# Performance work log

Hardware: AMD Instinct MI355X
Metric: run time of the kernel (lower is better)

## Reference

```python
import jax, jax.numpy as jnp
import numpy as np

CURV_BOUNDS = (-2.0, 2.0)
THRESH = 0.01   # |k| below this -> Euclidean branch
EPS = 1e-5

B, S, D = 4, 2048, 512


def setup_inputs() -> dict:
    key = jax.random.key(0)
    ks = jax.random.split(key, 8)
    x = jax.random.normal(ks[0], (B, S, D), jnp.float32)
    sc = 1.0 / np.sqrt(D)  # ~ nn.Linear default init scale
    Wq = jax.random.uniform(ks[1], (D, D), jnp.float32, -sc, sc)
    bq = jax.random.uniform(ks[2], (D,), jnp.float32, -sc, sc)
    Wk = jax.random.uniform(ks[3], (D, D), jnp.float32, -sc, sc)
    bk = jax.random.uniform(ks[4], (D,), jnp.float32, -sc, sc)
    Wv = jax.random.uniform(ks[5], (D, D), jnp.float32, -sc, sc)
    bv = jax.random.uniform(ks[6], (D,), jnp.float32, -sc, sc)
    curvature_raw = jnp.float32(0.5)   # init_curvature
    temperature = jnp.float32(1.0)
    mask = jnp.triu(jnp.ones((S, S), dtype=bool), 1)  # causal: True = masked out
    return {"x": x, "Wq": Wq, "bq": bq, "Wk": Wk, "bk": bk, "Wv": Wv,
            "bv": bv, "curvature_raw": curvature_raw,
            "temperature": temperature, "mask": mask}


def _curvature(raw):
    k_min, k_max = CURV_BOUNDS
    return k_min + (k_max - k_min) * (jnp.tanh(raw) + 1.0) / 2.0


def _project(u, k):
    # project_to_manifold: identity (euclid), Poincare-ball clip (k<0), sphere renorm (k>0)
    n = jnp.sqrt(jnp.sum(u * u, axis=-1, keepdims=True) + 1e-12)
    absk = jnp.abs(k)
    sk = jnp.sqrt(jnp.maximum(absk, EPS))
    max_norm = (1.0 - 1e-3) / sk                      # ball radius 1/sqrt(|k|)
    u_hyp = u * jnp.minimum(1.0, max_norm / n)
    u_sph = u / (n * sk)                              # sphere radius 1/sqrt(k)
    return jnp.where(absk < THRESH, u, jnp.where(k < 0, u_hyp, u_sph))


def reference(x, Wq, bq, Wk, bk, Wv, bv, curvature_raw, temperature, mask):
    k = _curvature(curvature_raw)
    q = x @ Wq.T + bq
    kk = x @ Wk.T + bk
    v = x @ Wv.T + bv
    qm = _project(q, k)
    km = _project(kk, k)

    # pairwise quantities without materializing [B,S,S,D]
    dots = jnp.einsum('bid,bjd->bij', qm, km)         # [B,S,S]
    qn2 = jnp.sum(qm * qm, axis=-1)                   # [B,S]
    kn2 = jnp.sum(km * km, axis=-1)                   # [B,S]
    diff2 = jnp.maximum(qn2[:, :, None] + kn2[:, None, :] - 2.0 * dots, 0.0)

    absk = jnp.abs(k)
    sk = jnp.sqrt(jnp.maximum(absk, EPS))

    d_euc = jnp.sqrt(diff2 + 1e-12)
    # hyperbolic (Poincare ball, c=|k|): acosh(1 + 2c|x-y|^2 / ((1-c|x|^2)(1-c|y|^2))) / sqrt(c)
    denom = jnp.maximum((1.0 - absk * qn2)[:, :, None] * (1.0 - absk * kn2)[:, None, :], EPS)
    arg = 1.0 + 2.0 * absk * diff2 / denom
    d_hyp = jnp.arccosh(jnp.maximum(arg, 1.0 + 1e-7)) / sk
    # spherical (radius 1/sqrt(k)): arccos(k * <x,y>) / sqrt(k)
    cosang = jnp.clip(absk * dots, -1.0 + 1e-7, 1.0 - 1e-7)
    d_sph = jnp.arccos(cosang) / sk

    dist = jnp.where(absk < THRESH, d_euc, jnp.where(k < 0, d_hyp, d_sph))

    scores = -dist / (temperature + 1e-8)
    scores = jnp.where(mask[None, :, :], -jnp.inf, scores)
    attention = jax.nn.softmax(scores, axis=-1)       # [B,S,S]
    output = jnp.einsum('bij,bjd->bid', attention, v) # [B,S,D]
    return output, attention
```

## Files before the change

kernel.cpp:

```cpp
#include <hip/hip_runtime.h>
#include <hip/hip_bf16.h>
#include <math.h>

typedef unsigned short u16;
typedef float float4e __attribute__((ext_vector_type(4)));
typedef short short8 __attribute__((ext_vector_type(8)));
typedef unsigned short ushort8 __attribute__((ext_vector_type(8)));
typedef unsigned short u16x4 __attribute__((ext_vector_type(4)));

#define SEQ 2048
#define DIM 512
#define NB  4

__device__ __forceinline__ float bf2f(u16 h) {
    return __uint_as_float(((unsigned)h) << 16);
}
__device__ __forceinline__ u16 f2bf(float f) {
    __hip_bfloat16 h = __float2bfloat16(f);
    return *reinterpret_cast<u16*>(&h);
}
__device__ __forceinline__ float curv_of(float raw) {
    return -2.0f + 2.0f * (tanhf(raw) + 1.0f);
}
__device__ __forceinline__ void gl_lds16(const u16* g, u16* lds) {
    __builtin_amdgcn_global_load_lds(
        (const __attribute__((address_space(1))) unsigned int*)g,
        (__attribute__((address_space(3))) unsigned int*)lds, 16, 0, 0);
}

__global__ __launch_bounds__(256) void cvt_all_kernel(
    const float* __restrict__ x, const float* __restrict__ Wq,
    const float* __restrict__ Wk, const float* __restrict__ Wv,
    u16* __restrict__ x_bf, u16* __restrict__ Wcat, float* __restrict__ lsum)
{
    const int n_x = NB * SEQ * DIM, n_w = DIM * DIM;
    int gid = blockIdx.x * 256 + threadIdx.x;
    if (gid < NB * SEQ) lsum[gid] = 0.f;
    int i4 = gid * 4;
    if (i4 < n_x) {
        float4 v = *(const float4*)&x[i4];
        u16x4 h = {f2bf(v.x), f2bf(v.y), f2bf(v.z), f2bf(v.w)};
        *(u16x4*)&x_bf[i4] = h;
    } else if (i4 < n_x + 3 * n_w) {
        int j = i4 - n_x;
        const float* W = (j < n_w) ? Wq : (j < 2 * n_w ? Wk : Wv);
        int off = j % n_w;
        float4 v = *(const float4*)&W[off];
        u16x4 h = {f2bf(v.x), f2bf(v.y), f2bf(v.z), f2bf(v.w)};
        *(u16x4*)&Wcat[j] = h;
    }
}

__global__ __launch_bounds__(256, 2) void gemm_qkv_kernel(
    const u16* __restrict__ A, const u16* __restrict__ Bt,
    u16* __restrict__ C, u16* __restrict__ vT,
    const float* __restrict__ bq, const float* __restrict__ bk, const float* __restrict__ bv)
{
    const int lda = 512, ldb = 512, ldc = 1536;
    int bn = blockIdx.x, bm = blockIdx.y;

    __shared__ __align__(16) u16 As[128 * 64];
    __shared__ __align__(16) u16 Bs[128 * 64];

    int t = threadIdx.x, wave = t >> 6, lane = t & 63;
    int wr = wave >> 1, wc = wave & 1;
    int lrow = lane & 15, quad = lane >> 4;
    int srow = lane >> 3, sc8 = lane & 7;

    const u16* Ab = A + (size_t)(bm * 128) * lda;
    const u16* Bb = Bt + (size_t)(bn * 128) * ldb;

    float4e acc[4][4];
#pragma unroll
    for (int i = 0; i < 4; i++)
#pragma unroll
        for (int j = 0; j < 4; j++) acc[i][j] = (float4e){0.f, 0.f, 0.f, 0.f};

    for (int kt = 0; kt < 8; ++kt) {
        int k0 = kt << 6;
        __syncthreads();
#pragma unroll
        for (int h = 0; h < 4; ++h) {
            int q = wave * 4 + h;
            int row = q * 8 + srow;
            int c = sc8 ^ (row & 7);
            gl_lds16(Ab + (size_t)row * lda + k0 + c * 8, &As[q * 512]);
            gl_lds16(Bb + (size_t)row * ldb + k0 + c * 8, &Bs[q * 512]);
        }
        __syncthreads();
#pragma unroll
        for (int kk = 0; kk < 2; ++kk) {
            short8 af[4], bfr[4];
#pragma unroll
            for (int im = 0; im < 4; im++) {
                int R = wr * 64 + im * 16 + lrow;
                af[im] = *(const short8*)&As[R * 64 + (((kk * 4 + quad) ^ (R & 7)) * 8)];
            }
#pragma unroll
            for (int in = 0; in < 4; in++) {
                int R = wc * 64 + in * 16 + lrow;
                bfr[in] = *(const short8*)&Bs[R * 64 + (((kk * 4 + quad) ^ (R & 7)) * 8)];
            }
#pragma unroll
            for (int im = 0; im < 4; im++)
#pragma unroll
                for (int in = 0; in < 4; in++)
                    acc[im][in] = __builtin_amdgcn_mfma_f32_16x16x32_bf16(af[im], bfr[in], acc[im][in], 0, 0, 0);
        }
    }

#pragma unroll
    for (int in = 0; in < 4; in++) {
        int gj = bn * 128 + wc * 64 + in * 16 + lrow;
        float bias = (gj < 512) ? bq[gj] : (gj < 1024 ? bk[gj - 512] : bv[gj - 1024]);
#pragma unroll
        for (int im = 0; im < 4; im++) {
            int gi0 = bm * 128 + wr * 64 + im * 16 + quad * 4;
            u16x4 pack;
#pragma unroll
            for (int r = 0; r < 4; r++) {
                u16 hv = f2bf(acc[im][in][r] + bias);
                C[(size_t)(gi0 + r) * ldc + gj] = hv;
                pack[r] = hv;
            }
            if (gj >= 1024) {
                int bb = gi0 >> 11, s = gi0 & 2047;
                *(u16x4*)&vT[((size_t)bb * DIM + (gj - 1024)) * SEQ + s] = pack;
            }
        }
    }
}

__global__ __launch_bounds__(256, 4) void gemm_scores_kernel(
    const u16* __restrict__ qm, const u16* __restrict__ km,
    u16* __restrict__ attnH,
    float* __restrict__ lsum,
    const float* __restrict__ qn2v, const float* __restrict__ kn2v,
    const float* __restrict__ curvp, const float* __restrict__ tempp)
{
    const int lda = 512, ldb = 512, ldc = SEQ;
    int bn = blockIdx.x, bm = blockIdx.y, b = blockIdx.z;
    if (bn > 2 * bm + 1) return;

    __shared__ __align__(16) u16 As[128 * 64];
    __shared__ __align__(16) u16 Bs[64 * 64];

    int t = threadIdx.x, wave = t >> 6, lane = t & 63;
    int wr = wave >> 1, wc = wave & 1;
    int lrow = lane & 15, quad = lane >> 4;
    int srow = lane >> 3, sc8 = lane & 7;

    const u16* Ab = qm + (size_t)b * SEQ * DIM + (size_t)(bm * 128) * lda;
    const u16* Bb = km + (size_t)b * SEQ * DIM + (size_t)(bn * 64) * ldb;

    float4e acc[4][2];
#pragma unroll
    for (int i = 0; i < 4; i++)
#pragma unroll
        for (int j = 0; j < 2; j++) acc[i][j] = (float4e){0.f, 0.f, 0.f, 0.f};

    for (int kt = 0; kt < 8; ++kt) {
        int k0 = kt << 6;
        __syncthreads();
#pragma unroll
        for (int h = 0; h < 4; ++h) {
            int q = wave * 4 + h;
            int row = q * 8 + srow;
            int c = sc8 ^ (row & 7);
            gl_lds16(Ab + (size_t)row * lda + k0 + c * 8, &As[q * 512]);
        }
#pragma unroll
        for (int h = 0; h < 2; ++h) {
            int q = wave * 2 + h;
            int row = q * 8 + srow;
            int c = sc8 ^ (row & 7);
            gl_lds16(Bb + (size_t)row * ldb + k0 + c * 8, &Bs[q * 512]);
        }
        __syncthreads();
#pragma unroll
        for (int kk = 0; kk < 2; ++kk) {
            short8 af[4], bfr[2];
#pragma unroll
            for (int im = 0; im < 4; im++) {
                int R = wr * 64 + im * 16 + lrow;
                af[im] = *(const short8*)&As[R * 64 + (((kk * 4 + quad) ^ (R & 7)) * 8)];
            }
#pragma unroll
            for (int in = 0; in < 2; in++) {
                int R = wc * 32 + in * 16 + lrow;
                bfr[in] = *(const short8*)&Bs[R * 64 + (((kk * 4 + quad) ^ (R & 7)) * 8)];
            }
#pragma unroll
            for (int im = 0; im < 4; im++)
#pragma unroll
                for (int in = 0; in < 2; in++)
                    acc[im][in] = __builtin_amdgcn_mfma_f32_16x16x32_bf16(af[im], bfr[in], acc[im][in], 0, 0, 0);
        }
    }

    float kv = curv_of(curvp[0]);
    float absk = fabsf(kv);
    float sk = sqrtf(fmaxf(absk, 1e-5f));
    float invT = 1.0f / (tempp[0] + 1e-8f);
    float Cexp = -1.4426950408889634f * invT;
    u16* Cb = attnH + (size_t)b * SEQ * SEQ;

    float psum[4][4];
#pragma unroll
    for (int im = 0; im < 4; im++)
#pragma unroll
        for (int r = 0; r < 4; r++) psum[im][r] = 0.f;

    float kn[2];
#pragma unroll
    for (int in = 0; in < 2; in++)
        kn[in] = kn2v[b * SEQ + bn * 64 + wc * 32 + in * 16 + lrow];

#pragma unroll
    for (int im = 0; im < 4; im++) {
#pragma unroll
        for (int r = 0; r < 4; r++) {
            int gi = bm * 128 + wr * 64 + im * 16 + quad * 4 + r;
            float qn = qn2v[b * SEQ + gi];
#pragma unroll
            for (int in = 0; in < 2; in++) {
                int gj = bn * 64 + wc * 32 + in * 16 + lrow;
                float dot = acc[im][in][r];
                float diff2 = fmaxf(qn + kn[in] - 2.f * dot, 0.f);
                float dist;
                if (absk < 0.01f) {
                    dist = sqrtf(diff2 + 1e-12f);
                } else if (kv < 0.f) {
                    float denom = fmaxf((1.f - absk * qn) * (1.f - absk * kn[in]), 1e-5f);
                    float arg = fmaxf(1.f + 2.f * absk * diff2 / denom, 1.f + 1e-7f);
                    dist = acoshf(arg) / sk;
                } else {
                    float c = fminf(fmaxf(absk * dot, -1.f + 1e-7f), 1.f - 1e-7f);
                    dist = acosf(c) / sk;
                }
                float e = (gj <= gi) ? exp2f(dist * Cexp) : 0.f;
                Cb[(size_t)gi * ldc + gj] = f2bf(e);
                psum[im][r] += e;
            }
        }
    }
#pragma unroll
    for (int im = 0; im < 4; im++)
#pragma unroll
        for (int r = 0; r < 4; r++) {
            float v = psum[im][r];
            v += __shfl_xor(v, 1);
            v += __shfl_xor(v, 2);
            v += __shfl_xor(v, 4);
            v += __shfl_xor(v, 8);
            if (lrow == 0) {
                int gi = bm * 128 + wr * 64 + im * 16 + quad * 4 + r;
                atomicAdd(&lsum[b * SEQ + gi], v);
            }
        }
}

__global__ __launch_bounds__(256, 8) void gemm_pv_kernel(
    const u16* __restrict__ attnH, const u16* __restrict__ vT,
    float* __restrict__ out, const float* __restrict__ lsum)
{
    const int lda = SEQ, ldb = SEQ, ldc = DIM;
    int bn = blockIdx.x, bm = blockIdx.y, b = blockIdx.z;

    __shared__ __align__(16) u16 As[64 * 64];
    __shared__ __align__(16) u16 Bs[64 * 64];

    int t = threadIdx.x, wave = t >> 6, lane = t & 63;
    int wr = wave >> 1, wc = wave & 1;
    int lrow = lane & 15, quad = lane >> 4;
    int srow = lane >> 3, sc = lane & 7;

    const u16* Ab = attnH + (size_t)b * SEQ * SEQ + (size_t)(bm * 64) * lda;
    const u16* Bb = vT + (size_t)b * DIM * SEQ + (size_t)(bn * 64) * ldb;

    float4e acc[2][2];
#pragma unroll
    for (int i = 0; i < 2; i++)
#pragma unroll
        for (int j = 0; j < 2; j++) acc[i][j] = (float4e){0.f, 0.f, 0.f, 0.f};

    for (int kt = 0; kt <= bm; ++kt) {
        int k0 = kt << 6;
        __syncthreads();
#pragma unroll
        for (int h = 0; h < 2; ++h) {
            int q = wave * 2 + h;
            int row = q * 8 + srow;
            int c = sc ^ (row & 7);
            gl_lds16(Ab + (size_t)row * lda + k0 + c * 8, &As[q * 512]);
            gl_lds16(Bb + (size_t)row * ldb + k0 + c * 8, &Bs[q * 512]);
        }
        __syncthreads();
#pragma unroll
        for (int s = 0; s < 2; ++s) {
            short8 af[2], bfr[2];
#pragma unroll
            for (int im = 0; im < 2; im++) {
                int R = wr * 32 + im * 16 + lrow;
                af[im] = *(const short8*)&As[R * 64 + (((s * 4 + quad) ^ (R & 7)) * 8)];
            }
#pragma unroll
            for (int in = 0; in < 2; in++) {
                int R = wc * 32 + in * 16 + lrow;
                bfr[in] = *(const short8*)&Bs[R * 64 + (((s * 4 + quad) ^ (R & 7)) * 8)];
            }
#pragma unroll
            for (int im = 0; im < 2; im++)
#pragma unroll
                for (int in = 0; in < 2; in++)
                    acc[im][in] = __builtin_amdgcn_mfma_f32_16x16x32_bf16(af[im], bfr[in], acc[im][in], 0, 0, 0);
        }
    }

    float* Cb = out + (size_t)b * SEQ * DIM;
#pragma unroll
    for (int im = 0; im < 2; im++)
#pragma unroll
        for (int r = 0; r < 4; r++) {
            int gi = bm * 64 + wr * 32 + im * 16 + quad * 4 + r;
            float invl = 1.0f / lsum[b * SEQ + gi];
#pragma unroll
            for (int in = 0; in < 2; in++) {
                int gd = bn * 64 + wc * 32 + in * 16 + lrow;
                Cb[(size_t)gi * ldc + gd] = acc[im][in][r] * invl;
            }
        }
}

__global__ __launch_bounds__(256) void project_kernel(
    const u16* __restrict__ qkvh,
    u16* __restrict__ qm, u16* __restrict__ km,
    float* __restrict__ qn2, float* __restrict__ kn2,
    const float* __restrict__ curvp)
{
    int wave = threadIdx.x >> 6, lane = threadIdx.x & 63;
    int r = blockIdx.x * 4 + wave;
    float kv = curv_of(curvp[0]);
    float absk = fabsf(kv);
    float sk = sqrtf(fmaxf(absk, 1e-5f));

    const u16* qrow = qkvh + (size_t)r * 1536;
    ushort8 qh = *(const ushort8*)&qrow[lane * 8];
    ushort8 kh = *(const ushort8*)&qrow[512 + lane * 8];

    float qv[8], kw[8];
    float sq = 0.f, s2 = 0.f;
#pragma unroll
    for (int e = 0; e < 8; e++) {
        qv[e] = bf2f(qh[e]); sq += qv[e] * qv[e];
        kw[e] = bf2f(kh[e]); s2 += kw[e] * kw[e];
    }
#pragma unroll
    for (int off = 1; off < 64; off <<= 1) {
        sq += __shfl_xor(sq, off);
        s2 += __shfl_xor(s2, off);
    }

    float sclq, sclk;
    {
        float nq = sqrtf(sq + 1e-12f);
        float nk = sqrtf(s2 + 1e-12f);
        if (absk < 0.01f) { sclq = 1.f; sclk = 1.f; }
        else if (kv < 0.f) {
            float mx = (1.0f - 1e-3f) / sk;
            sclq = fminf(1.f, mx / nq);
            sclk = fminf(1.f, mx / nk);
        } else {
            sclq = 1.f / (nq * sk);
            sclk = 1.f / (nk * sk);
        }
    }
    if (lane == 0) {
        qn2[r] = sq * sclq * sclq;
        kn2[r] = s2 * sclk * sclk;
    }
    ushort8 qo, ko;
#pragma unroll
    for (int e = 0; e < 8; e++) {
        qo[e] = f2bf(qv[e] * sclq);
        ko[e] = f2bf(kw[e] * sclk);
    }
    *(ushort8*)&qm[(size_t)r * 512 + lane * 8] = qo;
    *(ushort8*)&km[(size_t)r * 512 + lane * 8] = ko;
}

__global__ __launch_bounds__(256) void norm_attn_kernel(
    const u16* __restrict__ attnH, const float* __restrict__ lsum,
    float* __restrict__ attnF)
{
    int i = blockIdx.x, b = blockIdx.y, t = threadIdx.x;
    float inv = 1.0f / lsum[b * SEQ + i];
    const u16* rowh = attnH + ((size_t)b * SEQ + i) * SEQ;
    float* row = attnF + ((size_t)b * SEQ + i) * SEQ;
    int L = i + 1;
    int j0 = t * 8;
    float4 lo, hi;
    if (j0 + 8 <= L) {
        ushort8 h = *(const ushort8*)&rowh[j0];
        lo.x = bf2f(h[0]) * inv; lo.y = bf2f(h[1]) * inv;
        lo.z = bf2f(h[2]) * inv; lo.w = bf2f(h[3]) * inv;
        hi.x = bf2f(h[4]) * inv; hi.y = bf2f(h[5]) * inv;
        hi.z = bf2f(h[6]) * inv; hi.w = bf2f(h[7]) * inv;
    } else {
        float v[8];
#pragma unroll
        for (int e = 0; e < 8; e++)
            v[e] = (j0 + e < L) ? bf2f(rowh[j0 + e]) * inv : 0.f;
        lo = (float4){v[0], v[1], v[2], v[3]};
        hi = (float4){v[4], v[5], v[6], v[7]};
    }
    *(float4*)&row[j0] = lo;
    *(float4*)&row[j0 + 4] = hi;
}

extern "C" void kernel_launch(void* const* d_in, const int* in_sizes, int n_in,
                              void* d_out, int out_size, void* d_ws, size_t ws_size,
                              hipStream_t stream) {
    (void)in_sizes; (void)n_in; (void)out_size; (void)ws_size;

    const float* x    = (const float*)d_in[0];
    const float* Wq   = (const float*)d_in[1];
    const float* bq   = (const float*)d_in[2];
    const float* Wk   = (const float*)d_in[3];
    const float* bk   = (const float*)d_in[4];
    const float* Wv   = (const float*)d_in[5];
    const float* bv   = (const float*)d_in[6];
    const float* curv = (const float*)d_in[7];
    const float* temp = (const float*)d_in[8];

    float* out   = (float*)d_out;
    float* attnF = out + (size_t)NB * SEQ * DIM;

    char* ws = (char*)d_ws;
    u16*   x_bf  = (u16*)(ws + 0);
    u16*   Wcat  = (u16*)(ws + 8388608);
    u16*   qkvh  = (u16*)(ws + 9961472);
    u16*   qm    = (u16*)(ws + 35127296);
    u16*   km    = (u16*)(ws + 43515904);
    u16*   vT    = (u16*)(ws + 51904512);
    float* qn2   = (float*)(ws + 60293120);
    float* kn2   = (float*)(ws + 60325888);
    float* lsum  = (float*)(ws + 60358656);
    u16*   attnH = (u16*)(ws + 0);

    {
        int n_tot = (NB * SEQ * DIM + 3 * DIM * DIM) / 4;
        cvt_all_kernel<<<(n_tot + 255) / 256, 256, 0, stream>>>(x, Wq, Wk, Wv, x_bf, Wcat, lsum);
    }

    gemm_qkv_kernel<<<dim3(1536 / 128, 8192 / 128, 1), 256, 0, stream>>>(
        x_bf, Wcat, qkvh, vT, bq, bk, bv);

    project_kernel<<<NB * SEQ / 4, 256, 0, stream>>>(qkvh, qm, km, qn2, kn2, curv);

    gemm_scores_kernel<<<dim3(SEQ / 64, SEQ / 128, NB), 256, 0, stream>>>(
        qm, km, attnH, lsum, qn2, kn2, curv, temp);

    gemm_pv_kernel<<<dim3(DIM / 64, SEQ / 64, NB), 256, 0, stream>>>(
        attnH, vT, out, lsum);

    norm_attn_kernel<<<dim3(SEQ, NB), 256, 0, stream>>>(attnH, lsum, attnF);
}
```

Baseline: 239.9 us.

## Fuse projection into QKV/score GEMMs and attention normalization into PV kernel

Removes the separate project kernel. QKV GEMM epilogue now writes q and k directly and accumulates their row squared norms with atomics, and the manifold scaling is applied in the scores epilogue by rescaling the dot products. The score tile grows to 128x128 with occupancy hint reduced. The norm_attn kernel is folded into the PV kernel, which writes the normalized fp32 attention from LDS tiles and zero-fills the masked upper region. This trades extra launches and memory passes for atomics, a heavier PV epilogue and a changed rounding point (bf16 of unscaled q/k).

```diff
diff --git a/kernel.cpp b/kernel.cpp
--- a/kernel.cpp
+++ b/kernel.cpp
@@ -31,11 +31,12 @@
 __global__ __launch_bounds__(256) void cvt_all_kernel(
     const float* __restrict__ x, const float* __restrict__ Wq,
     const float* __restrict__ Wk, const float* __restrict__ Wv,
-    u16* __restrict__ x_bf, u16* __restrict__ Wcat, float* __restrict__ lsum)
+    u16* __restrict__ x_bf, u16* __restrict__ Wcat,
+    float* __restrict__ lsum, float* __restrict__ qn2r, float* __restrict__ kn2r)
 {
     const int n_x = NB * SEQ * DIM, n_w = DIM * DIM;
     int gid = blockIdx.x * 256 + threadIdx.x;
-    if (gid < NB * SEQ) lsum[gid] = 0.f;
+    if (gid < NB * SEQ) { lsum[gid] = 0.f; qn2r[gid] = 0.f; kn2r[gid] = 0.f; }
     int i4 = gid * 4;
     if (i4 < n_x) {
         float4 v = *(const float4*)&x[i4];
@@ -53,10 +54,11 @@
 
 __global__ __launch_bounds__(256, 2) void gemm_qkv_kernel(
     const u16* __restrict__ A, const u16* __restrict__ Bt,
-    u16* __restrict__ C, u16* __restrict__ vT,
-    const float* __restrict__ bq, const float* __restrict__ bk, const float* __restrict__ bv)
+    u16* __restrict__ qbuf, u16* __restrict__ kbuf, u16* __restrict__ vT,
+    const float* __restrict__ bq, const float* __restrict__ bk, const float* __restrict__ bv,
+    float* __restrict__ qn2r, float* __restrict__ kn2r)
 {
-    const int lda = 512, ldb = 512, ldc = 1536;
+    const int lda = 512, ldb = 512;
     int bn = blockIdx.x, bm = blockIdx.y;
 
     __shared__ __align__(16) u16 As[128 * 64];
@@ -109,6 +111,13 @@
         }
     }
 
+    int region = bn >> 2;
+    float nsum[4][4];
+#pragma unroll
+    for (int im = 0; im < 4; im++)
+#pragma unroll
+        for (int r = 0; r < 4; r++) nsum[im][r] = 0.f;
+
 #pragma unroll
     for (int in = 0; in < 4; in++) {
         int gj = bn * 128 + wc * 64 + in * 16 + lrow;
@@ -120,44 +129,63 @@
 #pragma unroll
             for (int r = 0; r < 4; r++) {
                 u16 hv = f2bf(acc[im][in][r] + bias);
-                C[(size_t)(gi0 + r) * ldc + gj] = hv;
                 pack[r] = hv;
-            }
-            if (gj >= 1024) {
+                if (region == 0) {
+                    qbuf[(size_t)(gi0 + r) * 512 + gj] = hv;
+                } else if (region == 1) {
+                    kbuf[(size_t)(gi0 + r) * 512 + (gj - 512)] = hv;
+                }
+                if (region < 2) { float vv = bf2f(hv); nsum[im][r] += vv * vv; }
+            }
+            if (region == 2) {
                 int bb = gi0 >> 11, s = gi0 & 2047;
                 *(u16x4*)&vT[((size_t)bb * DIM + (gj - 1024)) * SEQ + s] = pack;
             }
         }
     }
-}
-
-__global__ __launch_bounds__(256, 4) void gemm_scores_kernel(
-    const u16* __restrict__ qm, const u16* __restrict__ km,
-    u16* __restrict__ attnH,
-    float* __restrict__ lsum,
-    const float* __restrict__ qn2v, const float* __restrict__ kn2v,
+    if (region < 2) {
+        float* nrm = (region == 0) ? qn2r : kn2r;
+#pragma unroll
+        for (int im = 0; im < 4; im++)
+#pragma unroll
+            for (int r = 0; r < 4; r++) {
+                float v = nsum[im][r];
+                v += __shfl_xor(v, 1);
+                v += __shfl_xor(v, 2);
+                v += __shfl_xor(v, 4);
+                v += __shfl_xor(v, 8);
+                if (lrow == 0)
+                    atomicAdd(&nrm[bm * 128 + wr * 64 + im * 16 + quad * 4 + r], v);
+            }
+    }
+}
+
+__global__ __launch_bounds__(256, 2) void gemm_scores_kernel(
+    const u16* __restrict__ qbuf, const u16* __restrict__ kbuf,
+    u16* __restrict__ attnH, float* __restrict__ lsum,
+    const float* __restrict__ qn2r, const float* __restrict__ kn2r,
     const float* __restrict__ curvp, const float* __restrict__ tempp)
 {
     const int lda = 512, ldb = 512, ldc = SEQ;
     int bn = blockIdx.x, bm = blockIdx.y, b = blockIdx.z;
-    if (bn > 2 * bm + 1) return;
+    if (bn > bm) return;
 
     __shared__ __align__(16) u16 As[128 * 64];
-    __shared__ __align__(16) u16 Bs[64 * 64];
+    __shared__ __align__(16) u16 Bs[128 * 64];
 
     int t = threadIdx.x, wave = t >> 6, lane = t & 63;
     int wr = wave >> 1, wc = wave & 1;
     int lrow = lane & 15, quad = lane >> 4;
     int srow = lane >> 3, sc8 = lane & 7;
 
-    const u16* Ab = qm + (size_t)b * SEQ * DIM + (size_t)(bm * 128) * lda;
-    const u16* Bb = km + (size_t)b * SEQ * DIM + (size_t)(bn * 64) * ldb;
-
-    float4e acc[4][2];
+    const u16* Ab = qbuf + (size_t)(b * SEQ + bm * 128) * lda;
+    const u16* Bb = kbuf + (size_t)(b * SEQ + bn * 128) * ldb;
+
+    float4e acc[4][4];
 #pragma unroll
     for (int i = 0; i < 4; i++)
 #pragma unroll
-        for (int j = 0; j < 2; j++) acc[i][j] = (float4e){0.f, 0.f, 0.f, 0.f};
+        for (int j = 0; j < 4; j++) acc[i][j] = (float4e){0.f, 0.f, 0.f, 0.f};
 
     for (int kt = 0; kt < 8; ++kt) {
         int k0 = kt << 6;
@@ -168,32 +196,26 @@
             int row = q * 8 + srow;
             int c = sc8 ^ (row & 7);
             gl_lds16(Ab + (size_t)row * lda + k0 + c * 8, &As[q * 512]);
-        }
-#pragma unroll
-        for (int h = 0; h < 2; ++h) {
-            int q = wave * 2 + h;
-            int row = q * 8 + srow;
-            int c = sc8 ^ (row & 7);
             gl_lds16(Bb + (size_t)row * ldb + k0 + c * 8, &Bs[q * 512]);
         }
         __syncthreads();
 #pragma unroll
         for (int kk = 0; kk < 2; ++kk) {
-            short8 af[4], bfr[2];
+            short8 af[4], bfr[4];
 #pragma unroll
             for (int im = 0; im < 4; im++) {
                 int R = wr * 64 + im * 16 + lrow;
                 af[im] = *(const short8*)&As[R * 64 + (((kk * 4 + quad) ^ (R & 7)) * 8)];
             }
 #pragma unroll
-            for (int in = 0; in < 2; in++) {
-                int R = wc * 32 + in * 16 + lrow;
+            for (int in = 0; in < 4; in++) {
+                int R = wc * 64 + in * 16 + lrow;
                 bfr[in] = *(const short8*)&Bs[R * 64 + (((kk * 4 + quad) ^ (R & 7)) * 8)];
             }
 #pragma unroll
             for (int im = 0; im < 4; im++)
 #pragma unroll
-                for (int in = 0; in < 2; in++)
+                for (int in = 0; in < 4; in++)
                     acc[im][in] = __builtin_amdgcn_mfma_f32_16x16x32_bf16(af[im], bfr[in], acc[im][in], 0, 0, 0);
         }
     }
@@ -201,37 +223,46 @@
     float kv = curv_of(curvp[0]);
     float absk = fabsf(kv);
     float sk = sqrtf(fmaxf(absk, 1e-5f));
+    bool euc = (absk < 0.01f);
+    float mxn = (1.0f - 1e-3f) / sk;
     float invT = 1.0f / (tempp[0] + 1e-8f);
     float Cexp = -1.4426950408889634f * invT;
     u16* Cb = attnH + (size_t)b * SEQ * SEQ;
 
+    float sclk[4], knp[4];
+#pragma unroll
+    for (int in = 0; in < 4; in++) {
+        float kr = kn2r[b * SEQ + bn * 128 + wc * 64 + in * 16 + lrow];
+        float nk = sqrtf(kr + 1e-12f);
+        float s = euc ? 1.f : (kv < 0.f ? fminf(1.f, mxn / nk) : 1.f / (nk * sk));
+        sclk[in] = s; knp[in] = kr * s * s;
+    }
+
     float psum[4][4];
 #pragma unroll
     for (int im = 0; im < 4; im++)
 #pragma unroll
         for (int r = 0; r < 4; r++) psum[im][r] = 0.f;
-
-    float kn[2];
-#pragma unroll
-    for (int in = 0; in < 2; in++)
-        kn[in] = kn2v[b * SEQ + bn * 64 + wc * 32 + in * 16 + lrow];
 
 #pragma unroll
     for (int im = 0; im < 4; im++) {
 #pragma unroll
         for (int r = 0; r < 4; r++) {
             int gi = bm * 128 + wr * 64 + im * 16 + quad * 4 + r;
-            float qn = qn2v[b * SEQ + gi];
-#pragma unroll
-            for (int in = 0; in < 2; in++) {
-                int gj = bn * 64 + wc * 32 + in * 16 + lrow;
-                float dot = acc[im][in][r];
-                float diff2 = fmaxf(qn + kn[in] - 2.f * dot, 0.f);
+            float qr = qn2r[b * SEQ + gi];
+            float nq = sqrtf(qr + 1e-12f);
+            float sq_ = euc ? 1.f : (kv < 0.f ? fminf(1.f, mxn / nq) : 1.f / (nq * sk));
+            float qn = qr * sq_ * sq_;
+#pragma unroll
+            for (int in = 0; in < 4; in++) {
+                int gj = bn * 128 + wc * 64 + in * 16 + lrow;
+                float dot = acc[im][in][r] * sq_ * sclk[in];
+                float diff2 = fmaxf(qn + knp[in] - 2.f * dot, 0.f);
                 float dist;
-                if (absk < 0.01f) {
+                if (euc) {
                     dist = sqrtf(diff2 + 1e-12f);
                 } else if (kv < 0.f) {
-                    float denom = fmaxf((1.f - absk * qn) * (1.f - absk * kn[in]), 1e-5f);
+                    float denom = fmaxf((1.f - absk * qn) * (1.f - absk * knp[in]), 1e-5f);
                     float arg = fmaxf(1.f + 2.f * absk * diff2 / denom, 1.f + 1e-7f);
                     dist = acoshf(arg) / sk;
                 } else {
@@ -260,9 +291,10 @@
         }
 }
 
-__global__ __launch_bounds__(256, 8) void gemm_pv_kernel(
+__global__ __launch_bounds__(256, 4) void gemm_pv_kernel(
     const u16* __restrict__ attnH, const u16* __restrict__ vT,
-    float* __restrict__ out, const float* __restrict__ lsum)
+    float* __restrict__ out, float* __restrict__ attnF,
+    const float* __restrict__ lsum)
 {
     const int lda = SEQ, ldb = SEQ, ldc = DIM;
     int bn = blockIdx.x, bm = blockIdx.y, b = blockIdx.z;
@@ -277,6 +309,18 @@
 
     const u16* Ab = attnH + (size_t)b * SEQ * SEQ + (size_t)(bm * 64) * lda;
     const u16* Bb = vT + (size_t)b * DIM * SEQ + (size_t)(bn * 64) * ldb;
+    float* attnFb = attnF + (size_t)b * SEQ * SEQ;
+
+    {
+        int r = t >> 2, c4 = t & 3;
+        float4 z = (float4){0.f, 0.f, 0.f, 0.f};
+        for (int kt = bm + 1; kt < 32; ++kt)
+            if ((kt & 7) == bn) {
+                float* dst = attnFb + (size_t)(bm * 64 + r) * SEQ + kt * 64 + c4 * 16;
+                ((float4*)dst)[0] = z; ((float4*)dst)[1] = z;
+                ((float4*)dst)[2] = z; ((float4*)dst)[3] = z;
+            }
+    }
 
     float4e acc[2][2];
 #pragma unroll
@@ -315,6 +359,22 @@
                 for (int in = 0; in < 2; in++)
                     acc[im][in] = __builtin_amdgcn_mfma_f32_16x16x32_bf16(af[im], bfr[in], acc[im][in], 0, 0, 0);
         }
+        if ((kt & 7) == bn) {
+            int r = t >> 2, c4 = t & 3;
+            int gi = bm * 64 + r;
+            float invl = 1.0f / lsum[b * SEQ + gi];
+            const u16* src = &As[r * 64];
+            int j0 = c4 * 2;
+            ushort8 u0 = *(const ushort8*)&src[(j0 ^ (r & 7)) * 8];
+            ushort8 u1 = *(const ushort8*)&src[((j0 + 1) ^ (r & 7)) * 8];
+            float* dst = attnFb + (size_t)gi * SEQ + kt * 64 + c4 * 16;
+            float4 f0 = {bf2f(u0[0]) * invl, bf2f(u0[1]) * invl, bf2f(u0[2]) * invl, bf2f(u0[3]) * invl};
+            float4 f1 = {bf2f(u0[4]) * invl, bf2f(u0[5]) * invl, bf2f(u0[6]) * invl, bf2f(u0[7]) * invl};
+            float4 f2 = {bf2f(u1[0]) * invl, bf2f(u1[1]) * invl, bf2f(u1[2]) * invl, bf2f(u1[3]) * invl};
+            float4 f3 = {bf2f(u1[4]) * invl, bf2f(u1[5]) * invl, bf2f(u1[6]) * invl, bf2f(u1[7]) * invl};
+            ((float4*)dst)[0] = f0; ((float4*)dst)[1] = f1;
+            ((float4*)dst)[2] = f2; ((float4*)dst)[3] = f3;
+        }
     }
 
     float* Cb = out + (size_t)b * SEQ * DIM;
@@ -330,92 +390,6 @@
                 Cb[(size_t)gi * ldc + gd] = acc[im][in][r] * invl;
             }
         }
-}
-
-__global__ __launch_bounds__(256) void project_kernel(
-    const u16* __restrict__ qkvh,
-    u16* __restrict__ qm, u16* __restrict__ km,
-    float* __restrict__ qn2, float* __restrict__ kn2,
-    const float* __restrict__ curvp)
-{
-    int wave = threadIdx.x >> 6, lane = threadIdx.x & 63;
-    int r = blockIdx.x * 4 + wave;
-    float kv = curv_of(curvp[0]);
-    float absk = fabsf(kv);
-    float sk = sqrtf(fmaxf(absk, 1e-5f));
-
-    const u16* qrow = qkvh + (size_t)r * 1536;
-    ushort8 qh = *(const ushort8*)&qrow[lane * 8];
-    ushort8 kh = *(const ushort8*)&qrow[512 + lane * 8];
-
-    float qv[8], kw[8];
-    float sq = 0.f, s2 = 0.f;
-#pragma unroll
-    for (int e = 0; e < 8; e++) {
-        qv[e] = bf2f(qh[e]); sq += qv[e] * qv[e];
-        kw[e] = bf2f(kh[e]); s2 += kw[e] * kw[e];
-    }
-#pragma unroll
-    for (int off = 1; off < 64; off <<= 1) {
-        sq += __shfl_xor(sq, off);
-        s2 += __shfl_xor(s2, off);
-    }
-
-    float sclq, sclk;
-    {
-        float nq = sqrtf(sq + 1e-12f);
-        float nk = sqrtf(s2 + 1e-12f);
-        if (absk < 0.01f) { sclq = 1.f; sclk = 1.f; }
-        else if (kv < 0.f) {
-            float mx = (1.0f - 1e-3f) / sk;
-            sclq = fminf(1.f, mx / nq);
-            sclk = fminf(1.f, mx / nk);
-        } else {
-            sclq = 1.f / (nq * sk);
-            sclk = 1.f / (nk * sk);
-        }
-    }
-    if (lane == 0) {
-        qn2[r] = sq * sclq * sclq;
-        kn2[r] = s2 * sclk * sclk;
-    }
-    ushort8 qo, ko;
-#pragma unroll
-    for (int e = 0; e < 8; e++) {
-        qo[e] = f2bf(qv[e] * sclq);
-        ko[e] = f2bf(kw[e] * sclk);
-    }
-    *(ushort8*)&qm[(size_t)r * 512 + lane * 8] = qo;
-    *(ushort8*)&km[(size_t)r * 512 + lane * 8] = ko;
-}
-
-__global__ __launch_bounds__(256) void norm_attn_kernel(
-    const u16* __restrict__ attnH, const float* __restrict__ lsum,
-    float* __restrict__ attnF)
-{
-    int i = blockIdx.x, b = blockIdx.y, t = threadIdx.x;
-    float inv = 1.0f / lsum[b * SEQ + i];
-    const u16* rowh = attnH + ((size_t)b * SEQ + i) * SEQ;
-    float* row = attnF + ((size_t)b * SEQ + i) * SEQ;
-    int L = i + 1;
-    int j0 = t * 8;
-    float4 lo, hi;
-    if (j0 + 8 <= L) {
-        ushort8 h = *(const ushort8*)&rowh[j0];
-        lo.x = bf2f(h[0]) * inv; lo.y = bf2f(h[1]) * inv;
-        lo.z = bf2f(h[2]) * inv; lo.w = bf2f(h[3]) * inv;
-        hi.x = bf2f(h[4]) * inv; hi.y = bf2f(h[5]) * inv;
-        hi.z = bf2f(h[6]) * inv; hi.w = bf2f(h[7]) * inv;
-    } else {
-        float v[8];
-#pragma unroll
-        for (int e = 0; e < 8; e++)
-            v[e] = (j0 + e < L) ? bf2f(rowh[j0 + e]) * inv : 0.f;
-        lo = (float4){v[0], v[1], v[2], v[3]};
-        hi = (float4){v[4], v[5], v[6], v[7]};
-    }
-    *(float4*)&row[j0] = lo;
-    *(float4*)&row[j0 + 4] = hi;
 }
 
 extern "C" void kernel_launch(void* const* d_in, const int* in_sizes, int n_in,
@@ -439,30 +413,26 @@
     char* ws = (char*)d_ws;
     u16*   x_bf  = (u16*)(ws + 0);
     u16*   Wcat  = (u16*)(ws + 8388608);
-    u16*   qkvh  = (u16*)(ws + 9961472);
-    u16*   qm    = (u16*)(ws + 35127296);
-    u16*   km    = (u16*)(ws + 43515904);
-    u16*   vT    = (u16*)(ws + 51904512);
-    float* qn2   = (float*)(ws + 60293120);
-    float* kn2   = (float*)(ws + 60325888);
-    float* lsum  = (float*)(ws + 60358656);
     u16*   attnH = (u16*)(ws + 0);
+    u16*   qbuf  = (u16*)(ws + 33554432);
+    u16*   kbuf  = (u16*)(ws + 41943040);
+    u16*   vT    = (u16*)(ws + 50331648);
+    float* qn2r  = (float*)(ws + 58720256);
+    float* kn2r  = (float*)(ws + 58753024);
+    float* lsum  = (float*)(ws + 58785792);
 
     {
         int n_tot = (NB * SEQ * DIM + 3 * DIM * DIM) / 4;
-        cvt_all_kernel<<<(n_tot + 255) / 256, 256, 0, stream>>>(x, Wq, Wk, Wv, x_bf, Wcat, lsum);
+        cvt_all_kernel<<<(n_tot + 255) / 256, 256, 0, stream>>>(
+            x, Wq, Wk, Wv, x_bf, Wcat, lsum, qn2r, kn2r);
     }
 
     gemm_qkv_kernel<<<dim3(1536 / 128, 8192 / 128, 1), 256, 0, stream>>>(
-        x_bf, Wcat, qkvh, vT, bq, bk, bv);
-
-    project_kernel<<<NB * SEQ / 4, 256, 0, stream>>>(qkvh, qm, km, qn2, kn2, curv);
-
-    gemm_scores_kernel<<<dim3(SEQ / 64, SEQ / 128, NB), 256, 0, stream>>>(
-        qm, km, attnH, lsum, qn2, kn2, curv, temp);
+        x_bf, Wcat, qbuf, kbuf, vT, bq, bk, bv, qn2r, kn2r);
+
+    gemm_scores_kernel<<<dim3(SEQ / 128, SEQ / 128, NB), 256, 0, stream>>>(
+        qbuf, kbuf, attnH, lsum, qn2r, kn2r, curv, temp);
 
     gemm_pv_kernel<<<dim3(DIM / 64, SEQ / 64, NB), 256, 0, stream>>>(
-        attnH, vT, out, lsum);
-
-    norm_attn_kernel<<<dim3(SEQ, NB), 256, 0, stream>>>(attnH, lsum, attnF);
-}
+        attnH, vT, out, attnF, lsum);
+}
```

Result: slower. 276.0 us (+15.0%).
